# Kernel optimization log

Measured on AMD Instinct MI355X. Metric: run time of the kernel, lower is better.

The kernel has to match this reference:

```python
import jax, jax.numpy as jnp
import numpy as np

ALPHABET = 8
DIM = 128
SEQ_LEN = 8192
POWER_ITERS = 200


def setup_inputs() -> dict:
    key = jax.random.key(0)
    k1, k2, k3 = jax.random.split(key, 3)
    return {
        "Kraus_op_re": jax.random.uniform(k1, (ALPHABET, DIM, DIM), dtype=jnp.float32),
        "Kraus_op_im": jax.random.uniform(k2, (ALPHABET, DIM, DIM), dtype=jnp.float32),
        "sequence": jax.random.randint(k3, (SEQ_LEN,), 0, ALPHABET),
    }


def _leading_eig(K):
    # K: [A, d, d] complex. Power iteration on the transfer map and its adjoint.
    d = K.shape[-1]
    Kc = K.conj()

    def body_r(rhor, _):
        # rhov = sum_x K_x @ rhor @ K_x^H
        rhov = jnp.einsum("aij,jk,alk->il", K, rhor, Kc)
        mu = jnp.trace(rhov).real
        return rhov / mu.astype(rhov.dtype), None

    rhor, _ = jax.lax.scan(body_r, jnp.eye(d, dtype=K.dtype) / d, None, length=POWER_ITERS)

    def body_l(carry, _):
        rhol, _ = carry
        # rhov = sum_x K_x^H @ rhol @ K_x
        rhov = jnp.einsum("aji,jk,akl->il", Kc, rhol, K)
        mu = jnp.trace(rhov).real
        return (rhov / mu.astype(rhov.dtype), mu), None

    (rhol, mu), _ = jax.lax.scan(
        body_l, (jnp.eye(d, dtype=K.dtype), jnp.asarray(1.0, jnp.float32)), None, length=POWER_ITERS
    )
    return rhor, rhol, mu


def reference(Kraus_op_re, Kraus_op_im, sequence):
    K = Kraus_op_re.astype(jnp.complex64) + 1j * Kraus_op_im.astype(jnp.complex64)
    rhor, rhol, lam = _leading_eig(K)
    # normalize so that trace(rho @ rhol) == 1
    rho0 = rhor / jnp.trace(rhor @ rhol).real.astype(rhor.dtype)
    Kn = K / jnp.sqrt(lam).astype(K.dtype)  # Kraus ops rescaled by sqrt(leading eigenvalue)
    L = sequence.shape[0]

    def step(carry, inp):
        rho, logp = carry
        i, x = inp
        Kx = Kn[x]
        rho = Kx @ rho @ Kx.conj().T
        px = jnp.where(i == L - 1, jnp.trace(rho @ rhol).real, jnp.trace(rho).real)
        logp = logp - jnp.log2(px)
        rho = rho / px.astype(rho.dtype)
        return (rho, logp), None

    (_, log_p), _ = jax.lax.scan(
        step, (rho0, jnp.asarray(0.0, jnp.float32)), (jnp.arange(L), sequence)
    )
    return log_p[None]  # matches torch.tensor([0.0]) accumulator shape (1,)
```

## Files before the change

### kernel.cpp

```cpp
#include <hip/hip_runtime.h>

typedef unsigned int u32;
typedef unsigned short u16;
typedef __attribute__((ext_vector_type(4))) float f32x4;
typedef __attribute__((ext_vector_type(8))) short s16x8;
typedef __attribute__((ext_vector_type(4))) u32 u32x4;

#define DIMN 128
#define MATN (DIMN*DIMN)
#define NA 8
#define LSEQ 8192
#define NTOK (LSEQ/2)
#define PITERS 4
#define S1SH 5
#define S2SH 6
#define CHSH 7
#define P2SH 8
#define GCH 256
#define GLG 16

struct WS {
  u16 *Kb, *P2b, *rho, *nodes0, *nodes1, *rootR, *rootI;
  int *tok, *E0, *E1, *Eroot;
  float *trbuf;
  float *out;
};

__device__ __forceinline__ u16 f2bf(float x){
  u32 u = __float_as_uint(x);
  u32 r = (u + 0x7FFFu + ((u >> 16) & 1u)) >> 16;
  return (u16)r;
}
__device__ __forceinline__ float bf2f(u16 u){ return __uint_as_float(((u32)u) << 16); }
__device__ __forceinline__ u32 cvtpk(float lo, float hi){
  u32 r; asm("v_cvt_pk_bf16_f32 %0, %1, %2" : "=v"(r) : "v"(lo), "v"(hi)); return r;
}
__device__ __forceinline__ s16x8 negi(s16x8 v){
  return __builtin_bit_cast(s16x8, __builtin_bit_cast(u32x4, v) ^ 0x80008000u);
}
__device__ __forceinline__ int swz16(int maj, int b){
  return maj*256 + (((((b >> 4) + maj*5) & 15) << 4) | (b & 15));
}
__device__ __forceinline__ void cfma2(float2& c, float2 a, float2 b){
  c.x = fmaf(a.x, b.x, c.x); c.x = fmaf(-a.y, b.y, c.x);
  c.y = fmaf(a.x, b.y, c.y); c.y = fmaf(a.y, b.x, c.y);
}
template<int CA, int CB>
__device__ __forceinline__ void cmfma(s16x8 a_r, s16x8 a_i, s16x8 b_r, s16x8 b_i,
                                      f32x4& qr, f32x4& qi){
  s16x8 t1 = (CA ^ CB) ? a_i : negi(a_i);
  s16x8 t2 = CB ? negi(a_r) : a_r;
  s16x8 t3 = CA ? negi(a_i) : a_i;
  qr = __builtin_amdgcn_mfma_f32_16x16x32_bf16(a_r, b_r, qr, 0,0,0);
  qr = __builtin_amdgcn_mfma_f32_16x16x32_bf16(t1,  b_i, qr, 0,0,0);
  qi = __builtin_amdgcn_mfma_f32_16x16x32_bf16(t2,  b_i, qi, 0,0,0);
  qi = __builtin_amdgcn_mfma_f32_16x16x32_bf16(t3,  b_r, qi, 0,0,0);
}

__global__ __launch_bounds__(256) void k_kbinit(const float* Kre, const float* Kim,
                                                const int* seq, WS w){
  __shared__ u16 Lr[32][36], Li[32][36];
  int blk = blockIdx.x, x = blk >> 4, tile = blk & 15;
  int row0 = (tile>>2)*32, col0 = (tile&3)*32;
  int t = threadIdx.x;
  { int r = t>>3, cch = t&7;
    size_t off = (size_t)x*MATN + (size_t)(row0+r)*128 + col0 + cch*4;
    float4 vr = *(const float4*)(Kre + off);
    float4 vi = *(const float4*)(Kim + off);
    Lr[r][cch*4+0] = f2bf(vr.x); Lr[r][cch*4+1] = f2bf(vr.y);
    Lr[r][cch*4+2] = f2bf(vr.z); Lr[r][cch*4+3] = f2bf(vr.w);
    Li[r][cch*4+0] = f2bf(vi.x); Li[r][cch*4+1] = f2bf(vi.y);
    Li[r][cch*4+2] = f2bf(vi.z); Li[r][cch*4+3] = f2bf(vi.w);
  }
  __syncthreads();
  u16* b = w.Kb + (size_t)x*4*MATN;
  { int r = t>>3, cch = t&7;
    *(uint2*)&b[(row0+r)*128 + col0 + cch*4]        = *(uint2*)&Lr[r][cch*4];
    *(uint2*)&b[MATN + (row0+r)*128 + col0 + cch*4] = *(uint2*)&Li[r][cch*4];
  }
  { int c = t>>3, rch = t&7;
    ushort4 vr, vi;
    vr.x = Lr[rch*4+0][c]; vr.y = Lr[rch*4+1][c];
    vr.z = Lr[rch*4+2][c]; vr.w = Lr[rch*4+3][c];
    vi.x = Li[rch*4+0][c]; vi.y = Li[rch*4+1][c];
    vi.z = Li[rch*4+2][c]; vi.w = Li[rch*4+3][c];
    *(ushort4*)&b[2*MATN + (col0+c)*128 + row0 + rch*4] = vr;
    *(ushort4*)&b[3*MATN + (col0+c)*128 + row0 + rch*4] = vi;
  }
  int gid = blockIdx.x*256 + t, gsz = gridDim.x*256;
  for (int i = gid; i < NTOK; i += gsz)
    w.tok[i] = seq[2*i+1]*NA + seq[2*i];
  for (int i = gid; i < 4*MATN; i += gsz){
    int plane = (i >> 14) & 1, rem = i & (MATN-1);
    u16 v = (plane == 0 && (rem >> 7) == (rem & 127)) ? f2bf(1.f) : (u16)0;
    w.rho[i] = v;
  }
  if (gid < 32) w.trbuf[gid] = 0.f;
}

__global__ __launch_bounds__(256) void k_p2(const float* Kre, const float* Kim, WS w){
  __shared__ float2 As[16][33], Bs[16][33];
  int blk = blockIdx.x, mat = blk >> 4, tile = blk & 15;
  int a = mat >> 3, b = mat & 7;
  int row0 = (tile>>2)*32, col0 = (tile&3)*32;
  int t = threadIdx.x, ti = t & 15, tk = t >> 4;
  float2 acc[4] = {{0,0},{0,0},{0,0},{0,0}};
  for (int k0 = 0; k0 < 128; k0 += 16){
    { int r = t >> 4, kk = t & 15;
      size_t i0 = (size_t)a*MATN + (size_t)(row0+r)*DIMN + k0+kk;
      size_t i1 = i0 + 16*DIMN;
      As[kk][r]    = make_float2(Kre[i0], Kim[i0]);
      As[kk][r+16] = make_float2(Kre[i1], Kim[i1]); }
    { int kk = t >> 5, c = t & 31;
      size_t i0 = (size_t)b*MATN + (size_t)(k0+kk)*DIMN + col0+c;
      size_t i1 = i0 + 8*DIMN;
      Bs[kk][c]   = make_float2(Kre[i0], Kim[i0]);
      Bs[kk+8][c] = make_float2(Kre[i1], Kim[i1]); }
    __syncthreads();
    #pragma unroll
    for (int jj = 0; jj < 16; jj++){
      float2 a0 = As[jj][ti], a1 = As[jj][ti+16];
      float2 b0 = Bs[jj][tk], b1 = Bs[jj][tk+16];
      cfma2(acc[0], a0, b0); cfma2(acc[1], a0, b1);
      cfma2(acc[2], a1, b0); cfma2(acc[3], a1, b1);
    }
    __syncthreads();
  }
  u16* Lr = (u16*)As; u16* Li = (u16*)Bs;
  const float sc = 1.f/(1<<P2SH);
  Lr[ti*36+tk]         = f2bf(acc[0].x*sc); Li[ti*36+tk]         = f2bf(acc[0].y*sc);
  Lr[ti*36+tk+16]      = f2bf(acc[1].x*sc); Li[ti*36+tk+16]      = f2bf(acc[1].y*sc);
  Lr[(ti+16)*36+tk]    = f2bf(acc[2].x*sc); Li[(ti+16)*36+tk]    = f2bf(acc[2].y*sc);
  Lr[(ti+16)*36+tk+16] = f2bf(acc[3].x*sc); Li[(ti+16)*36+tk+16] = f2bf(acc[3].y*sc);
  __syncthreads();
  u16* base = w.P2b + (size_t)mat*4*MATN;
  { int r = t>>3, cch = t&7;
    *(uint2*)&base[(row0+r)*128 + col0 + cch*4]        = *(uint2*)&Lr[r*36 + cch*4];
    *(uint2*)&base[MATN + (row0+r)*128 + col0 + cch*4] = *(uint2*)&Li[r*36 + cch*4];
  }
  { int c = t>>3, rch = t&7;
    ushort4 vr, vi;
    vr.x = Lr[(rch*4+0)*36 + c]; vr.y = Lr[(rch*4+1)*36 + c];
    vr.z = Lr[(rch*4+2)*36 + c]; vr.w = Lr[(rch*4+3)*36 + c];
    vi.x = Li[(rch*4+0)*36 + c]; vi.y = Li[(rch*4+1)*36 + c];
    vi.z = Li[(rch*4+2)*36 + c]; vi.w = Li[(rch*4+3)*36 + c];
    *(ushort4*)&base[2*MATN + (col0+c)*128 + row0 + rch*4] = vr;
    *(ushort4*)&base[3*MATN + (col0+c)*128 + row0 + rch*4] = vi;
  }
}

__device__ __forceinline__ void loadA(const u16* Ar, const u16* Ai,
    int wr, int l15, int hi, s16x8 (&fr)[4][2], s16x8 (&fi)[4][2]){
  #pragma unroll
  for (int kk = 0; kk < 4; kk++){
    int kb = kk*32 + hi*8;
    #pragma unroll
    for (int m = 0; m < 2; m++){
      int r = wr + m*16 + l15;
      fr[kk][m] = *(const s16x8*)(Ar + r*128 + kb);
      fi[kk][m] = *(const s16x8*)(Ai + r*128 + kb);
    }
  }
}
__device__ __forceinline__ void ccomputeR(const s16x8 (&fr)[4][2], const s16x8 (&fi)[4][2],
    const char* Pr, const char* Pi, f32x4 (&qr)[2][4], f32x4 (&qi)[2][4],
    int wc, int l15, int hi){
  #pragma unroll
  for (int m=0;m<2;m++)
    #pragma unroll
    for (int n=0;n<4;n++){ qr[m][n] = (f32x4){0,0,0,0}; qi[m][n] = (f32x4){0,0,0,0}; }
  #pragma unroll
  for (int kk = 0; kk < 4; kk++){
    int kb = kk*32 + hi*8;
    #pragma unroll
    for (int n=0;n<4;n++){
      int c = wc + n*16 + l15;
      int o = swz16(c, kb*2);
      s16x8 b_r = *(const s16x8*)(Pr + o);
      s16x8 b_i = *(const s16x8*)(Pi + o);
      #pragma unroll
      for (int m=0;m<2;m++)
        cmfma<0,0>(fr[kk][m], fi[kk][m], b_r, b_i, qr[m][n], qi[m][n]);
    }
  }
}
__device__ __forceinline__ void pwrite16(char* Pr, char* Pi,
    f32x4 (&qr)[2][4], f32x4 (&qi)[2][4], float sc, int t){
  int wv = t>>6, lane = t&63, l15 = lane&15, hi = lane>>4;
  int wr = (wv>>1)*32, wc = (wv&1)*64;
  #pragma unroll
  for (int m=0;m<2;m++)
    #pragma unroll
    for (int n=0;n<4;n++){
      int c = wc + n*16 + l15, r0 = wr + m*16 + hi*4;
      uint2 pr, pi;
      pr.x = cvtpk(qr[m][n][0]*sc, qr[m][n][1]*sc);
      pr.y = cvtpk(qr[m][n][2]*sc, qr[m][n][3]*sc);
      pi.x = cvtpk(qi[m][n][0]*sc, qi[m][n][1]*sc);
      pi.y = cvtpk(qi[m][n][2]*sc, qi[m][n][3]*sc);
      int o = swz16(c, r0*2);
      *(uint2*)(Pr + o) = pr;
      *(uint2*)(Pi + o) = pi;
    }
}
__device__ __forceinline__ int renorm_to(char* Pr, char* Pi, float* red,
    f32x4 (&qr)[2][4], f32x4 (&qi)[2][4], int t){
  int wv = t>>6, lane = t&63;
  float lm = 0.f;
  #pragma unroll
  for (int m=0;m<2;m++)
    #pragma unroll
    for (int n=0;n<4;n++)
      #pragma unroll
      for (int j=0;j<4;j++)
        lm = fmaxf(lm, fmaxf(fabsf(qr[m][n][j]), fabsf(qi[m][n][j])));
  #pragma unroll
  for (int o = 32; o > 0; o >>= 1) lm = fmaxf(lm, __shfl_xor(lm, o, 64));
  if (lane == 0) red[wv] = lm;
  __syncthreads();
  float mx = 0.f;
  #pragma unroll
  for (int i = 0; i < 8; i++) mx = fmaxf(mx, red[i]);
  int e = 0; if (mx > 0.f) frexpf(mx, &e);
  pwrite16(Pr, Pi, qr, qi, ldexpf(1.f, -e), t);
  return e;
}
__device__ __forceinline__ void stage_cols16(const u16* gr, const u16* gi,
                                             char* Pr, char* Pi, int t){
  #pragma unroll
  for (int i = 0; i < 4; i++){
    int chunk = t + i*512;
    int c = chunk >> 4, rr = chunk & 15;
    int o = swz16(c, rr*16);
    *(uint4*)(Pr + o) = *(const uint4*)(gr + c*128 + rr*8);
    *(uint4*)(Pi + o) = *(const uint4*)(gi + c*128 + rr*8);
  }
}
__device__ __forceinline__ void write_node16(u16* dr, u16* di,
    const char* Pr, const char* Pi, bool rowLayout, int t){
  if (!rowLayout){
    #pragma unroll
    for (int i = 0; i < 4; i++){
      int chunk = t + i*512;
      int c = chunk >> 4, rr = chunk & 15;
      int o = swz16(c, rr*16);
      *(uint4*)(dr + c*128 + rr*8) = *(const uint4*)(Pr + o);
      *(uint4*)(di + c*128 + rr*8) = *(const uint4*)(Pi + o);
    }
  } else {
    for (int idx = t; idx < MATN; idx += 512){
      int r = idx >> 7, c = idx & 127;
      int o = swz16(c, r*2);
      dr[idx] = *(const u16*)(Pr + o);
      di[idx] = *(const u16*)(Pi + o);
    }
  }
}

__global__ __launch_bounds__(512,1) void k_chain(WS w){
  __shared__ __align__(16) char P0r[32768];
  __shared__ __align__(16) char P0i[32768];
  __shared__ __align__(16) char P1r[32768];
  __shared__ __align__(16) char P1i[32768];
  __shared__ float red[8];
  int p = blockIdx.x, t = threadIdx.x;
  int wv = t>>6, lane = t&63, l15 = lane&15, hi = lane>>4;
  int wr = (wv>>1)*32, wc = (wv&1)*64;
  char *PrC = P0r, *PiC = P0i, *PrN = P1r, *PiN = P1i;
  int tok0 = w.tok[p*GLG];
  const u16* b0 = w.P2b + (size_t)tok0*4*MATN;
  stage_cols16(b0 + 2*MATN, b0 + 3*MATN, PrC, PiC, t);
  s16x8 A1r[4][2], A1i[4][2], A2r[4][2], A2i[4][2];
  { const u16* tb = w.P2b + (size_t)w.tok[p*GLG + 1]*4*MATN;
    loadA(tb, tb + MATN, wr, l15, hi, A1r, A1i); }
  f32x4 qr[2][4], qi[2][4];
  int eLast = 0;
  __syncthreads();
  #pragma unroll 1
  for (int s = 1; s < GLG; s += 2){
    if (s+1 < GLG){
      const u16* tb = w.P2b + (size_t)w.tok[p*GLG + s+1]*4*MATN;
      loadA(tb, tb + MATN, wr, l15, hi, A2r, A2i);
    }
    ccomputeR(A1r, A1i, PrC, PiC, qr, qi, wc, l15, hi);
    if (s < GLG-1) pwrite16(PrN, PiN, qr, qi, 1.f/(1<<CHSH), t);
    else eLast = renorm_to(PrN, PiN, red, qr, qi, t);
    __syncthreads();
    { char* x = PrC; PrC = PrN; PrN = x; x = PiC; PiC = PiN; PiN = x; }
    if (s+1 < GLG){
      if (s+2 < GLG){
        const u16* tb = w.P2b + (size_t)w.tok[p*GLG + s+2]*4*MATN;
        loadA(tb, tb + MATN, wr, l15, hi, A1r, A1i);
      }
      ccomputeR(A2r, A2i, PrC, PiC, qr, qi, wc, l15, hi);
      if (s+1 < GLG-1) pwrite16(PrN, PiN, qr, qi, 1.f/(1<<CHSH), t);
      else eLast = renorm_to(PrN, PiN, red, qr, qi, t);
      __syncthreads();
      { char* x = PrC; PrC = PrN; PrN = x; x = PiC; PiC = PiN; PiN = x; }
    }
  }
  u16* slot = w.nodes0 + (size_t)p*2*MATN;
  write_node16(slot, slot + MATN, PrC, PiC, (p & 3) != 0, t);
  if (t == 0) w.E0[p] = P2SH*GLG + CHSH*(GLG-2) + eLast;
}

__global__ __launch_bounds__(512,1) void k_level(WS w, int srcIs0, int isRoot){
  __shared__ __align__(16) char P0r[32768];
  __shared__ __align__(16) char P0i[32768];
  __shared__ __align__(16) char P1r[32768];
  __shared__ __align__(16) char P1i[32768];
  __shared__ float red[8];
  int p = blockIdx.x, t = threadIdx.x;
  int wv = t>>6, lane = t&63, l15 = lane&15, hi = lane>>4;
  int wr = (wv>>1)*32, wc = (wv&1)*64;
  char *PrC = P0r, *PiC = P0i, *PrN = P1r, *PiN = P1i;
  const u16* src = srcIs0 ? w.nodes0 : w.nodes1;
  u16* dst       = srcIs0 ? w.nodes1 : w.nodes0;
  const int* Es  = srcIs0 ? w.E0 : w.E1;
  int* Ed        = srcIs0 ? w.E1 : w.E0;
  const u16* B = src + (size_t)(4*p)*2*MATN;
  stage_cols16(B, B + MATN, PrC, PiC, t);
  s16x8 A1r[4][2], A1i[4][2], A2r[4][2], A2i[4][2];
  { const u16* A = src + (size_t)(4*p+1)*2*MATN;
    loadA(A, A + MATN, wr, l15, hi, A1r, A1i); }
  int E = Es[4*p] + Es[4*p+1] + Es[4*p+2] + Es[4*p+3];
  f32x4 qr[2][4], qi[2][4];
  __syncthreads();
  { const u16* A = src + (size_t)(4*p+2)*2*MATN;
    loadA(A, A + MATN, wr, l15, hi, A2r, A2i); }
  ccomputeR(A1r, A1i, PrC, PiC, qr, qi, wc, l15, hi);
  E += renorm_to(PrN, PiN, red, qr, qi, t);
  __syncthreads();
  { char* x = PrC; PrC = PrN; PrN = x; x = PiC; PiC = PiN; PiN = x; }
  { const u16* A = src + (size_t)(4*p+3)*2*MATN;
    loadA(A, A + MATN, wr, l15, hi, A1r, A1i); }
  ccomputeR(A2r, A2i, PrC, PiC, qr, qi, wc, l15, hi);
  E += renorm_to(PrN, PiN, red, qr, qi, t);
  __syncthreads();
  { char* x = PrC; PrC = PrN; PrN = x; x = PiC; PiC = PiN; PiN = x; }
  ccomputeR(A1r, A1i, PrC, PiC, qr, qi, wc, l15, hi);
  E += renorm_to(PrN, PiN, red, qr, qi, t);
  __syncthreads();
  { char* x = PrC; PrC = PrN; PrN = x; x = PiC; PiC = PiN; PiN = x; }
  u16* slot = dst + (size_t)p*2*MATN;
  write_node16(slot, slot + MATN, PrC, PiC, ((p & 3) != 0) || isRoot, t);
  if (t == 0) Ed[p] = E;
}

__global__ __launch_bounds__(512,1) void k_pow(WS w, int par){
  __shared__ __align__(16) char Rr[32768];
  __shared__ __align__(16) char Ri[32768];
  __shared__ __align__(16) char Yr[32768];
  __shared__ __align__(16) char Yi[32768];
  int b = blockIdx.x, side = b >> 3, rb = b & 7;
  int t = threadIdx.x, wv = t>>6, lane = t&63, l15 = lane&15, hi = lane>>4;
  const u16* rhoS = w.rho + (size_t)((par*2 + side)*2)*MATN;
  stage_cols16(rhoS, rhoS + MATN, Rr, Ri, t);
  __syncthreads();
  { int x = wv;
    const u16* Ab = w.Kb + (size_t)(x*4 + (side ? 2 : 0))*MATN;
    const u16* Ar = Ab; const u16* Ai = Ab + MATN;
    f32x4 q1r[8], q1i[8];
    #pragma unroll
    for (int n=0;n<8;n++){ q1r[n] = (f32x4){0,0,0,0}; q1i[n] = (f32x4){0,0,0,0}; }
    #pragma unroll
    for (int kk = 0; kk < 4; kk++){
      int kb = kk*32 + hi*8;
      int r = rb*16 + l15;
      s16x8 a_r = *(const s16x8*)(Ar + r*128 + kb);
      s16x8 a_i = *(const s16x8*)(Ai + r*128 + kb);
      #pragma unroll
      for (int n=0;n<8;n++){
        int c = n*16 + l15;
        int o = swz16(c, kb*2);
        s16x8 b_r = *(const s16x8*)(Rr + o);
        s16x8 b_i = *(const s16x8*)(Ri + o);
        if (side == 0) cmfma<0,0>(a_r, a_i, b_r, b_i, q1r[n], q1i[n]);
        else           cmfma<1,0>(a_r, a_i, b_r, b_i, q1r[n], q1i[n]);
      }
    }
    const float sc = 1.f/(1<<S1SH);
    #pragma unroll
    for (int n=0;n<8;n++)
      #pragma unroll
      for (int q=0;q<4;q++){
        int lr = hi*4 + q, c = n*16 + l15;
        *(u16*)(Yr + x*4096 + swz16(lr, c*2)) = f2bf(q1r[n][q]*sc);
        *(u16*)(Yi + x*4096 + swz16(lr, c*2)) = f2bf(q1i[n][q]*sc);
      }
  }
  __syncthreads();
  { int c0 = wv*16, c = c0 + l15;
    f32x4 q2r = {0,0,0,0}, q2i = {0,0,0,0};
    #pragma unroll 2
    for (int x = 0; x < 8; x++){
      const u16* Bb = w.Kb + (size_t)(x*4 + (side ? 2 : 0))*MATN;
      const u16* Br = Bb; const u16* Bi = Bb + MATN;
      #pragma unroll
      for (int kk = 0; kk < 4; kk++){
        int kb = kk*32 + hi*8;
        s16x8 a_r = *(const s16x8*)(Yr + x*4096 + swz16(l15, kb*2));
        s16x8 a_i = *(const s16x8*)(Yi + x*4096 + swz16(l15, kb*2));
        s16x8 b_r = *(const s16x8*)(Br + c*128 + kb);
        s16x8 b_i = *(const s16x8*)(Bi + c*128 + kb);
        if (side == 0) cmfma<0,1>(a_r, a_i, b_r, b_i, q2r, q2i);
        else           cmfma<0,0>(a_r, a_i, b_r, b_i, q2r, q2i);
      }
    }
    const float sc = 1.f/(1<<S2SH);
    u16* Dr = w.rho + (size_t)(((par^1)*2 + side)*2)*MATN;
    u16* Di = Dr + MATN;
    int r0g = rb*16 + hi*4;
    uint2 pr, pi;
    pr.x = cvtpk(q2r[0]*sc, q2r[1]*sc); pr.y = cvtpk(q2r[2]*sc, q2r[3]*sc);
    pi.x = cvtpk(q2i[0]*sc, q2i[1]*sc); pi.y = cvtpk(q2i[2]*sc, q2i[3]*sc);
    *(uint2*)(Dr + c*128 + r0g) = pr;
    *(uint2*)(Di + c*128 + r0g) = pi;
    if (side == 1 && wv == rb){
      float tr = 0.f;
      #pragma unroll
      for (int q=0;q<4;q++) if (hi*4 + q == l15) tr += q2r[q]*sc;
      #pragma unroll
      for (int o = 32; o > 0; o >>= 1) tr += __shfl_xor(tr, o, 64);
      if (lane == 0) w.trbuf[par*16 + 8 + rb] = tr;
    }
  }
}

__global__ __launch_bounds__(512) void k_epi(WS w){
  __shared__ __align__(16) char T1r[32768];
  __shared__ __align__(16) char T1i[32768];
  int t = threadIdx.x, wv = t>>6, lane = t&63, l15 = lane&15, hi = lane>>4;
  int wr = (wv>>2)*64, wc = (wv&3)*32;
  f32x4 qr[4][2], qi[4][2];
  const u16* Ar = w.rho;
  const u16* Ai = Ar + MATN;
  #pragma unroll
  for (int m=0;m<4;m++)
    #pragma unroll
    for (int n=0;n<2;n++){ qr[m][n] = (f32x4){0,0,0,0}; qi[m][n] = (f32x4){0,0,0,0}; }
  #pragma unroll
  for (int kk = 0; kk < 4; kk++){
    int kb = kk*32 + hi*8;
    #pragma unroll
    for (int m=0;m<4;m++){
      int r = wr + m*16 + l15;
      s16x8 a_r = *(const s16x8*)(Ar + r*128 + kb);
      s16x8 a_i = *(const s16x8*)(Ai + r*128 + kb);
      #pragma unroll
      for (int n=0;n<2;n++){
        int c = wc + n*16 + l15;
        s16x8 b_r = *(const s16x8*)(w.rootR + c*128 + kb);
        s16x8 b_i = *(const s16x8*)(w.rootI + c*128 + kb);
        cmfma<0,0>(a_r, a_i, b_r, b_i, qr[m][n], qi[m][n]);
      }
    }
  }
  {
    const float sc = 1.f/(1<<CHSH);
    #pragma unroll
    for (int m=0;m<4;m++)
      #pragma unroll
      for (int n=0;n<2;n++){
        int c = wc + n*16 + l15, r0 = wr + m*16 + hi*4;
        uint2 pr, pi;
        pr.x = cvtpk(qr[m][n][0]*sc, qr[m][n][1]*sc);
        pr.y = cvtpk(qr[m][n][2]*sc, qr[m][n][3]*sc);
        pi.x = cvtpk(qi[m][n][0]*sc, qi[m][n][1]*sc);
        pi.y = cvtpk(qi[m][n][2]*sc, qi[m][n][3]*sc);
        int o = swz16(c, r0*2);
        *(uint2*)(T1r + o) = pr;
        *(uint2*)(T1i + o) = pi;
      }
  }
  __syncthreads();
  #pragma unroll
  for (int m=0;m<4;m++)
    #pragma unroll
    for (int n=0;n<2;n++){ qr[m][n] = (f32x4){0,0,0,0}; qi[m][n] = (f32x4){0,0,0,0}; }
  #pragma unroll
  for (int kk = 0; kk < 4; kk++){
    int kb = kk*32 + hi*8;
    #pragma unroll
    for (int m=0;m<4;m++){
      int r = wr + m*16 + l15;
      int o = swz16(r, kb*2);
      s16x8 a_r = *(const s16x8*)(T1r + o);
      s16x8 a_i = *(const s16x8*)(T1i + o);
      #pragma unroll
      for (int n=0;n<2;n++){
        int c = wc + n*16 + l15;
        s16x8 b_r = *(const s16x8*)(w.rootR + c*128 + kb);
        s16x8 b_i = *(const s16x8*)(w.rootI + c*128 + kb);
        cmfma<0,1>(a_r, a_i, b_r, b_i, qr[m][n], qi[m][n]);
      }
    }
  }
  __syncthreads();
  double* red = (double*)T1r;
  const u16* rlr = w.rho + (size_t)2*MATN;
  const u16* rli = rlr + MATN;
  double a1 = 0.0;
  #pragma unroll
  for (int m=0;m<4;m++)
    #pragma unroll
    for (int n=0;n<2;n++){
      int c = wc + n*16 + l15, r0 = wr + m*16 + hi*4;
      #pragma unroll
      for (int q=0;q<4;q++){
        int r = r0 + q;
        float lr = bf2f(rlr[r*128 + c]), li = bf2f(rli[r*128 + c]);
        a1 += (double)qr[m][n][q]*lr - (double)qi[m][n][q]*li;
      }
    }
  red[t] = a1; __syncthreads();
  for (int o = 256; o > 0; o >>= 1){ if (t < o) red[t] += red[t+o]; __syncthreads(); }
  double that = red[0]; __syncthreads();
  const u16* rrr = w.rho;
  const u16* rri = rrr + MATN;
  double a2 = 0.0;
  for (int idx = t; idx < MATN; idx += 512){
    int c = idx >> 7, r = idx & 127;
    float ar_ = bf2f(rrr[idx]), ai_ = bf2f(rri[idx]);
    float lr  = bf2f(rlr[r*128 + c]), li = bf2f(rli[r*128 + c]);
    a2 += (double)ar_*lr - (double)ai_*li;
  }
  red[t] = a2; __syncthreads();
  for (int o = 256; o > 0; o >>= 1){ if (t < o) red[t] += red[t+o]; __syncthreads(); }
  double trrl = red[0];
  if (t == 0){
    double T0 = 0.0, T1s = 0.0;
    for (int s = 0; s < 8; s++){ T0 += w.trbuf[8+s]; T1s += w.trbuf[16+8+s]; }
    double lam = ldexp(T1s / T0, S1SH + S2SH);
    double logp = (double)LSEQ * log2(lam) - 2.0*(double)w.Eroot[0] - (double)CHSH
                  - log2(fmax(that, 1e-300)) + log2(fmax(trrl, 1e-300));
    w.out[0] = (float)logp;
  }
}

static inline size_t aln256(size_t x){ return (x + 255) & ~(size_t)255; }

extern "C" void kernel_launch(void* const* d_in, const int* in_sizes, int n_in,
                              void* d_out, int out_size, void* d_ws, size_t ws_size,
                              hipStream_t stream){
  const float* Kre = (const float*)d_in[0];
  const float* Kim = (const float*)d_in[1];
  const int*   seq = (const int*)d_in[2];

  WS w{};
  char* p = (char*)d_ws;
  auto take = [&](size_t bytes)->char*{ char* r = p; p += aln256(bytes); return r; };
  w.Kb    = (u16*)take((size_t)NA*4*MATN*2);
  w.P2b   = (u16*)take((size_t)64*4*MATN*2);
  w.rho   = (u16*)take((size_t)8*MATN*2);
  w.nodes0= (u16*)take((size_t)GCH*2*MATN*2);
  w.nodes1= (u16*)take((size_t)(GCH/4)*2*MATN*2);
  w.tok   = (int*)take(NTOK*4);
  w.E0    = (int*)take(GCH*4);
  w.E1    = (int*)take(GCH*4);
  w.trbuf = (float*)take(32*4);
  w.out = (float*)d_out;
  w.rootR = w.nodes0; w.rootI = w.nodes0 + MATN;
  w.Eroot = w.E0;

  hipLaunchKernelGGL(k_kbinit, dim3(NA*16), dim3(256), 0, stream, Kre, Kim, seq, w);
  hipLaunchKernelGGL(k_p2, dim3(64*16), dim3(256), 0, stream, Kre, Kim, w);
  hipLaunchKernelGGL(k_chain, dim3(GCH), dim3(512), 0, stream, w);
  hipLaunchKernelGGL(k_level, dim3(64), dim3(512), 0, stream, w, 1, 0);
  hipLaunchKernelGGL(k_level, dim3(16), dim3(512), 0, stream, w, 0, 0);
  hipLaunchKernelGGL(k_level, dim3(4),  dim3(512), 0, stream, w, 1, 0);
  hipLaunchKernelGGL(k_level, dim3(1),  dim3(512), 0, stream, w, 0, 1);
  for (int k = 0; k < PITERS; k++)
    hipLaunchKernelGGL(k_pow, dim3(16), dim3(512), 0, stream, w, k & 1);
  hipLaunchKernelGGL(k_epi, dim3(1), dim3(512), 0, stream, w);
}
```

Measured before the change: 347.9 us.

## Compute pair products with MFMA and drop register prefetch for two blocks per CU

```diff
diff --git a/kernel.cpp b/kernel.cpp
--- a/kernel.cpp
+++ b/kernel.cpp
@@ -40,10 +40,6 @@
 }
 __device__ __forceinline__ int swz16(int maj, int b){
   return maj*256 + (((((b >> 4) + maj*5) & 15) << 4) | (b & 15));
-}
-__device__ __forceinline__ void cfma2(float2& c, float2 a, float2 b){
-  c.x = fmaf(a.x, b.x, c.x); c.x = fmaf(-a.y, b.y, c.x);
-  c.y = fmaf(a.x, b.y, c.y); c.y = fmaf(a.y, b.x, c.y);
 }
 template<int CA, int CB>
 __device__ __forceinline__ void cmfma(s16x8 a_r, s16x8 a_i, s16x8 b_r, s16x8 b_i,
@@ -98,80 +94,24 @@
   if (gid < 32) w.trbuf[gid] = 0.f;
 }
 
-__global__ __launch_bounds__(256) void k_p2(const float* Kre, const float* Kim, WS w){
-  __shared__ float2 As[16][33], Bs[16][33];
-  int blk = blockIdx.x, mat = blk >> 4, tile = blk & 15;
-  int a = mat >> 3, b = mat & 7;
-  int row0 = (tile>>2)*32, col0 = (tile&3)*32;
-  int t = threadIdx.x, ti = t & 15, tk = t >> 4;
-  float2 acc[4] = {{0,0},{0,0},{0,0},{0,0}};
-  for (int k0 = 0; k0 < 128; k0 += 16){
-    { int r = t >> 4, kk = t & 15;
-      size_t i0 = (size_t)a*MATN + (size_t)(row0+r)*DIMN + k0+kk;
-      size_t i1 = i0 + 16*DIMN;
-      As[kk][r]    = make_float2(Kre[i0], Kim[i0]);
-      As[kk][r+16] = make_float2(Kre[i1], Kim[i1]); }
-    { int kk = t >> 5, c = t & 31;
-      size_t i0 = (size_t)b*MATN + (size_t)(k0+kk)*DIMN + col0+c;
-      size_t i1 = i0 + 8*DIMN;
-      Bs[kk][c]   = make_float2(Kre[i0], Kim[i0]);
-      Bs[kk+8][c] = make_float2(Kre[i1], Kim[i1]); }
-    __syncthreads();
-    #pragma unroll
-    for (int jj = 0; jj < 16; jj++){
-      float2 a0 = As[jj][ti], a1 = As[jj][ti+16];
-      float2 b0 = Bs[jj][tk], b1 = Bs[jj][tk+16];
-      cfma2(acc[0], a0, b0); cfma2(acc[1], a0, b1);
-      cfma2(acc[2], a1, b0); cfma2(acc[3], a1, b1);
-    }
-    __syncthreads();
-  }
-  u16* Lr = (u16*)As; u16* Li = (u16*)Bs;
-  const float sc = 1.f/(1<<P2SH);
-  Lr[ti*36+tk]         = f2bf(acc[0].x*sc); Li[ti*36+tk]         = f2bf(acc[0].y*sc);
-  Lr[ti*36+tk+16]      = f2bf(acc[1].x*sc); Li[ti*36+tk+16]      = f2bf(acc[1].y*sc);
-  Lr[(ti+16)*36+tk]    = f2bf(acc[2].x*sc); Li[(ti+16)*36+tk]    = f2bf(acc[2].y*sc);
-  Lr[(ti+16)*36+tk+16] = f2bf(acc[3].x*sc); Li[(ti+16)*36+tk+16] = f2bf(acc[3].y*sc);
-  __syncthreads();
-  u16* base = w.P2b + (size_t)mat*4*MATN;
-  { int r = t>>3, cch = t&7;
-    *(uint2*)&base[(row0+r)*128 + col0 + cch*4]        = *(uint2*)&Lr[r*36 + cch*4];
-    *(uint2*)&base[MATN + (row0+r)*128 + col0 + cch*4] = *(uint2*)&Li[r*36 + cch*4];
-  }
-  { int c = t>>3, rch = t&7;
-    ushort4 vr, vi;
-    vr.x = Lr[(rch*4+0)*36 + c]; vr.y = Lr[(rch*4+1)*36 + c];
-    vr.z = Lr[(rch*4+2)*36 + c]; vr.w = Lr[(rch*4+3)*36 + c];
-    vi.x = Li[(rch*4+0)*36 + c]; vi.y = Li[(rch*4+1)*36 + c];
-    vi.z = Li[(rch*4+2)*36 + c]; vi.w = Li[(rch*4+3)*36 + c];
-    *(ushort4*)&base[2*MATN + (col0+c)*128 + row0 + rch*4] = vr;
-    *(ushort4*)&base[3*MATN + (col0+c)*128 + row0 + rch*4] = vi;
-  }
-}
-
-__device__ __forceinline__ void loadA(const u16* Ar, const u16* Ai,
-    int wr, int l15, int hi, s16x8 (&fr)[4][2], s16x8 (&fi)[4][2]){
+__device__ __forceinline__ void ccompute(const u16* Ar, const u16* Ai,
+    const char* Pr, const char* Pi, f32x4 (&qr)[2][4], f32x4 (&qi)[2][4], int t){
+  int wv = t>>6, lane = t&63, l15 = lane&15, hi = lane>>4;
+  int wr = (wv>>1)*32, wc = (wv&1)*64;
+  #pragma unroll
+  for (int m=0;m<2;m++)
+    #pragma unroll
+    for (int n=0;n<4;n++){ qr[m][n] = (f32x4){0,0,0,0}; qi[m][n] = (f32x4){0,0,0,0}; }
   #pragma unroll
   for (int kk = 0; kk < 4; kk++){
     int kb = kk*32 + hi*8;
-    #pragma unroll
-    for (int m = 0; m < 2; m++){
+    s16x8 a_r[2], a_i[2];
+    #pragma unroll
+    for (int m=0;m<2;m++){
       int r = wr + m*16 + l15;
-      fr[kk][m] = *(const s16x8*)(Ar + r*128 + kb);
-      fi[kk][m] = *(const s16x8*)(Ai + r*128 + kb);
-    }
-  }
-}
-__device__ __forceinline__ void ccomputeR(const s16x8 (&fr)[4][2], const s16x8 (&fi)[4][2],
-    const char* Pr, const char* Pi, f32x4 (&qr)[2][4], f32x4 (&qi)[2][4],
-    int wc, int l15, int hi){
-  #pragma unroll
-  for (int m=0;m<2;m++)
-    #pragma unroll
-    for (int n=0;n<4;n++){ qr[m][n] = (f32x4){0,0,0,0}; qi[m][n] = (f32x4){0,0,0,0}; }
-  #pragma unroll
-  for (int kk = 0; kk < 4; kk++){
-    int kb = kk*32 + hi*8;
+      a_r[m] = *(const s16x8*)(Ar + r*128 + kb);
+      a_i[m] = *(const s16x8*)(Ai + r*128 + kb);
+    }
     #pragma unroll
     for (int n=0;n<4;n++){
       int c = wc + n*16 + l15;
@@ -180,7 +120,7 @@
       s16x8 b_i = *(const s16x8*)(Pi + o);
       #pragma unroll
       for (int m=0;m<2;m++)
-        cmfma<0,0>(fr[kk][m], fi[kk][m], b_r, b_i, qr[m][n], qi[m][n]);
+        cmfma<0,0>(a_r[m], a_i[m], b_r, b_i, qr[m][n], qi[m][n]);
     }
   }
 }
@@ -257,62 +197,61 @@
   }
 }
 
-__global__ __launch_bounds__(512,1) void k_chain(WS w){
+__global__ __launch_bounds__(512) void k_p2m(WS w){
+  __shared__ __align__(16) char P0r[32768];
+  __shared__ __align__(16) char P0i[32768];
+  __shared__ __align__(16) char P1r[32768];
+  __shared__ __align__(16) char P1i[32768];
+  int blk = blockIdx.x, a = blk >> 3, b = blk & 7;
+  int t = threadIdx.x;
+  const u16* Bb = w.Kb + (size_t)(b*4 + 2)*MATN;
+  stage_cols16(Bb, Bb + MATN, P0r, P0i, t);
+  __syncthreads();
+  const u16* Ab = w.Kb + (size_t)(a*4)*MATN;
+  f32x4 qr[2][4], qi[2][4];
+  ccompute(Ab, Ab + MATN, P0r, P0i, qr, qi, t);
+  pwrite16(P1r, P1i, qr, qi, 1.f/(1<<P2SH), t);
+  __syncthreads();
+  u16* base = w.P2b + (size_t)blk*4*MATN;
+  write_node16(base + 2*MATN, base + 3*MATN, P1r, P1i, false, t);
+  write_node16(base, base + MATN, P1r, P1i, true, t);
+}
+
+__global__ __launch_bounds__(512,2) void k_chain(WS w){
   __shared__ __align__(16) char P0r[32768];
   __shared__ __align__(16) char P0i[32768];
   __shared__ __align__(16) char P1r[32768];
   __shared__ __align__(16) char P1i[32768];
   __shared__ float red[8];
   int p = blockIdx.x, t = threadIdx.x;
-  int wv = t>>6, lane = t&63, l15 = lane&15, hi = lane>>4;
-  int wr = (wv>>1)*32, wc = (wv&1)*64;
   char *PrC = P0r, *PiC = P0i, *PrN = P1r, *PiN = P1i;
   int tok0 = w.tok[p*GLG];
   const u16* b0 = w.P2b + (size_t)tok0*4*MATN;
   stage_cols16(b0 + 2*MATN, b0 + 3*MATN, PrC, PiC, t);
-  s16x8 A1r[4][2], A1i[4][2], A2r[4][2], A2i[4][2];
-  { const u16* tb = w.P2b + (size_t)w.tok[p*GLG + 1]*4*MATN;
-    loadA(tb, tb + MATN, wr, l15, hi, A1r, A1i); }
   f32x4 qr[2][4], qi[2][4];
   int eLast = 0;
   __syncthreads();
   #pragma unroll 1
-  for (int s = 1; s < GLG; s += 2){
-    if (s+1 < GLG){
-      const u16* tb = w.P2b + (size_t)w.tok[p*GLG + s+1]*4*MATN;
-      loadA(tb, tb + MATN, wr, l15, hi, A2r, A2i);
-    }
-    ccomputeR(A1r, A1i, PrC, PiC, qr, qi, wc, l15, hi);
+  for (int s = 1; s < GLG; s++){
+    const u16* tb = w.P2b + (size_t)w.tok[p*GLG + s]*4*MATN;
+    ccompute(tb, tb + MATN, PrC, PiC, qr, qi, t);
     if (s < GLG-1) pwrite16(PrN, PiN, qr, qi, 1.f/(1<<CHSH), t);
     else eLast = renorm_to(PrN, PiN, red, qr, qi, t);
     __syncthreads();
     { char* x = PrC; PrC = PrN; PrN = x; x = PiC; PiC = PiN; PiN = x; }
-    if (s+1 < GLG){
-      if (s+2 < GLG){
-        const u16* tb = w.P2b + (size_t)w.tok[p*GLG + s+2]*4*MATN;
-        loadA(tb, tb + MATN, wr, l15, hi, A1r, A1i);
-      }
-      ccomputeR(A2r, A2i, PrC, PiC, qr, qi, wc, l15, hi);
-      if (s+1 < GLG-1) pwrite16(PrN, PiN, qr, qi, 1.f/(1<<CHSH), t);
-      else eLast = renorm_to(PrN, PiN, red, qr, qi, t);
-      __syncthreads();
-      { char* x = PrC; PrC = PrN; PrN = x; x = PiC; PiC = PiN; PiN = x; }
-    }
   }
   u16* slot = w.nodes0 + (size_t)p*2*MATN;
   write_node16(slot, slot + MATN, PrC, PiC, (p & 3) != 0, t);
   if (t == 0) w.E0[p] = P2SH*GLG + CHSH*(GLG-2) + eLast;
 }
 
-__global__ __launch_bounds__(512,1) void k_level(WS w, int srcIs0, int isRoot){
+__global__ __launch_bounds__(512,2) void k_level(WS w, int srcIs0, int isRoot){
   __shared__ __align__(16) char P0r[32768];
   __shared__ __align__(16) char P0i[32768];
   __shared__ __align__(16) char P1r[32768];
   __shared__ __align__(16) char P1i[32768];
   __shared__ float red[8];
   int p = blockIdx.x, t = threadIdx.x;
-  int wv = t>>6, lane = t&63, l15 = lane&15, hi = lane>>4;
-  int wr = (wv>>1)*32, wc = (wv&1)*64;
   char *PrC = P0r, *PiC = P0i, *PrN = P1r, *PiN = P1i;
   const u16* src = srcIs0 ? w.nodes0 : w.nodes1;
   u16* dst       = srcIs0 ? w.nodes1 : w.nodes0;
@@ -320,28 +259,17 @@
   int* Ed        = srcIs0 ? w.E1 : w.E0;
   const u16* B = src + (size_t)(4*p)*2*MATN;
   stage_cols16(B, B + MATN, PrC, PiC, t);
-  s16x8 A1r[4][2], A1i[4][2], A2r[4][2], A2i[4][2];
-  { const u16* A = src + (size_t)(4*p+1)*2*MATN;
-    loadA(A, A + MATN, wr, l15, hi, A1r, A1i); }
   int E = Es[4*p] + Es[4*p+1] + Es[4*p+2] + Es[4*p+3];
   f32x4 qr[2][4], qi[2][4];
   __syncthreads();
-  { const u16* A = src + (size_t)(4*p+2)*2*MATN;
-    loadA(A, A + MATN, wr, l15, hi, A2r, A2i); }
-  ccomputeR(A1r, A1i, PrC, PiC, qr, qi, wc, l15, hi);
-  E += renorm_to(PrN, PiN, red, qr, qi, t);
-  __syncthreads();
-  { char* x = PrC; PrC = PrN; PrN = x; x = PiC; PiC = PiN; PiN = x; }
-  { const u16* A = src + (size_t)(4*p+3)*2*MATN;
-    loadA(A, A + MATN, wr, l15, hi, A1r, A1i); }
-  ccomputeR(A2r, A2i, PrC, PiC, qr, qi, wc, l15, hi);
-  E += renorm_to(PrN, PiN, red, qr, qi, t);
-  __syncthreads();
-  { char* x = PrC; PrC = PrN; PrN = x; x = PiC; PiC = PiN; PiN = x; }
-  ccomputeR(A1r, A1i, PrC, PiC, qr, qi, wc, l15, hi);
-  E += renorm_to(PrN, PiN, red, qr, qi, t);
-  __syncthreads();
-  { char* x = PrC; PrC = PrN; PrN = x; x = PiC; PiC = PiN; PiN = x; }
+  #pragma unroll 1
+  for (int j = 1; j < 4; j++){
+    const u16* A = src + (size_t)(4*p + j)*2*MATN;
+    ccompute(A, A + MATN, PrC, PiC, qr, qi, t);
+    E += renorm_to(PrN, PiN, red, qr, qi, t);
+    __syncthreads();
+    { char* x = PrC; PrC = PrN; PrN = x; x = PiC; PiC = PiN; PiN = x; }
+  }
   u16* slot = dst + (size_t)p*2*MATN;
   write_node16(slot, slot + MATN, PrC, PiC, ((p & 3) != 0) || isRoot, t);
   if (t == 0) Ed[p] = E;
@@ -564,7 +492,7 @@
   w.Eroot = w.E0;
 
   hipLaunchKernelGGL(k_kbinit, dim3(NA*16), dim3(256), 0, stream, Kre, Kim, seq, w);
-  hipLaunchKernelGGL(k_p2, dim3(64*16), dim3(256), 0, stream, Kre, Kim, w);
+  hipLaunchKernelGGL(k_p2m, dim3(64), dim3(512), 0, stream, w);
   hipLaunchKernelGGL(k_chain, dim3(GCH), dim3(512), 0, stream, w);
   hipLaunchKernelGGL(k_level, dim3(64), dim3(512), 0, stream, w, 1, 0);
   hipLaunchKernelGGL(k_level, dim3(16), dim3(512), 0, stream, w, 0, 0);
```

Result: faster. 310.0 us (-10.9%).
